# Performance work log

Hardware: AMD Instinct MI355X
Metric: run time of the kernel (lower is better)

Reference implementation:

```python
import jax, jax.numpy as jnp
import numpy as np


def setup_inputs() -> dict:
    key = jax.random.key(0)
    ka, kb = jax.random.split(key)
    a = jax.random.normal(ka, (16384, 3), dtype=jnp.float32)
    b = jax.random.normal(kb, (16384, 3), dtype=jnp.float32)
    return {"a": a, "b": b}


def reference(a, b):
    # Pairwise squared L2 via the expansion ||a-b||^2 = ||a||^2 + ||b||^2 - 2 a.b,
    # avoiding materializing the [N, M, D] diff tensor the torch code builds.
    a2 = jnp.sum(a * a, axis=-1)                      # [N]
    b2 = jnp.sum(b * b, axis=-1)                      # [M]
    cross = jnp.einsum("nd,md->nm", a, b)             # [N, M]
    d2 = a2[:, None] + b2[None, :] - 2.0 * cross       # [N, M]
    dist = jnp.sqrt(jnp.maximum(d2, 0.0))              # clamp for numerical safety
    min_dist = jnp.min(dist, axis=1)                   # [N] nearest-neighbor dist
    return jnp.sum(min_dist)
```

## Files before the change

kernel.cpp:

```cpp
#include <hip/hip_runtime.h>
#include <math.h>


#define NPTS 16384

typedef short s16x8 __attribute__((ext_vector_type(8)));
typedef unsigned int u32x4 __attribute__((ext_vector_type(4)));
typedef float f32x16 __attribute__((ext_vector_type(16)));

__device__ __forceinline__ unsigned short f2bf(float x) {
    unsigned u = __float_as_uint(x);
    u = u + 0x7FFFu + ((u >> 16) & 1u);
    return (unsigned short)(u >> 16);
}
__device__ __forceinline__ float bf2f(unsigned short h) {
    return __uint_as_float((unsigned)h << 16);
}
__device__ __forceinline__ unsigned pk(unsigned short lo, unsigned short hi) {
    return (unsigned)lo | ((unsigned)hi << 16);
}

__global__ __launch_bounds__(256)
void cd_packb_kernel(const float* __restrict__ b,
                     u32x4* __restrict__ bcmp) {
    const int i = blockIdx.x * 256 + threadIdx.x;
    const float x = b[3 * i + 0], y = b[3 * i + 1], z = b[3 * i + 2];
    const float n2 = fmaf(x, x, fmaf(y, y, z * z));
    const unsigned short hx = f2bf(x), hy = f2bf(y), hz = f2bf(z);
    const unsigned short thx = f2bf(-2.0f * bf2f(hx));
    const unsigned short thy = f2bf(-2.0f * bf2f(hy));
    const unsigned short thz = f2bf(-2.0f * bf2f(hz));
    const unsigned short tlx = f2bf(-2.0f * (x - bf2f(hx)));
    const unsigned short tly = f2bf(-2.0f * (y - bf2f(hy)));
    const unsigned short tlz = f2bf(-2.0f * (z - bf2f(hz)));
    const unsigned short n2h = f2bf(n2), n2l = f2bf(n2 - bf2f(n2h));
    bcmp[i] = (u32x4){ pk(thx, thy), pk(thz, tlx), pk(tly, tlz), pk(n2h, n2l) };
}

__device__ __forceinline__ s16x8 make_afrag(const float* __restrict__ a,
                                            int row, int khalf) {
    const float x = a[3 * row + 0];
    const float y = a[3 * row + 1];
    const float z = a[3 * row + 2];
    const float n2 = fmaf(x, x, fmaf(y, y, z * z));
    const unsigned short hx = f2bf(x), hy = f2bf(y), hz = f2bf(z);
    const unsigned short lx = f2bf(x - bf2f(hx));
    const unsigned short ly = f2bf(y - bf2f(hy));
    const unsigned short lz = f2bf(z - bf2f(hz));
    const unsigned short n2h = f2bf(n2);
    const unsigned short n2l = f2bf(n2 - bf2f(n2h));
    const unsigned short one = 0x3F80u;
    const s16x8 lo = {(short)hx, (short)hy, (short)hz, (short)hx,
                      (short)hy, (short)hz, (short)lx, (short)ly};
    const s16x8 hi = {(short)lz, (short)lx, (short)ly, (short)lz,
                      (short)n2h, (short)n2l, (short)one, (short)one};
    return khalf ? hi : lo;
}

__global__ __launch_bounds__(512, 4)
void cd_sweep_kernel(const float* __restrict__ a,
                     const u32x4* __restrict__ bcmp,
                     float* __restrict__ gmin) {
    __shared__ float red[8][64];
    const int tid   = threadIdx.x;
    const int lane  = tid & 63;
    const int wave  = tid >> 6;
    const int col   = lane & 31;
    const int khalf = lane >> 5;
    const int agroup = blockIdx.x >> 1;
    const int g      = blockIdx.x & 1;

    const s16x8 af0 = make_afrag(a, agroup * 64 + col, khalf);
    const s16x8 af1 = make_afrag(a, agroup * 64 + 32 + col, khalf);

    f32x16 best0, best1, zero;
    #pragma unroll
    for (int r = 0; r < 16; ++r) {
        best0[r] = 3.4028235e38f; best1[r] = 3.4028235e38f; zero[r] = 0.0f;
    }

    const unsigned Kone = 0x3F803F80u;
    const u32x4* bp = bcmp + g * 8192 + wave * 1024 + col;

    #define EXPAND(e, d)                           \
        e[0] = khalf ? d[1] : d[0];                \
        e[1] = khalf ? d[2] : d[1];                \
        e[2] = khalf ? Kone : d[2];                \
        e[3] = khalf ? d[3] : d[0];

    #pragma unroll 2
    for (int t = 0; t < 32; t += 2) {
        const u32x4 d0 = bp[(t + 0) * 32];
        const u32x4 d1 = bp[(t + 1) * 32];
        u32x4 e0, e1;
        EXPAND(e0, d0) EXPAND(e1, d1)
        {
            const f32x16 c0 = __builtin_amdgcn_mfma_f32_32x32x16_bf16(
                __builtin_bit_cast(s16x8, e0), af0, zero, 0, 0, 0);
            const f32x16 c1 = __builtin_amdgcn_mfma_f32_32x32x16_bf16(
                __builtin_bit_cast(s16x8, e1), af0, zero, 0, 0, 0);
            #pragma unroll
            for (int r = 0; r < 16; ++r)
                best0[r] = fminf(fminf(c0[r], c1[r]), best0[r]);
        }
        {
            const f32x16 c0 = __builtin_amdgcn_mfma_f32_32x32x16_bf16(
                __builtin_bit_cast(s16x8, e0), af1, zero, 0, 0, 0);
            const f32x16 c1 = __builtin_amdgcn_mfma_f32_32x32x16_bf16(
                __builtin_bit_cast(s16x8, e1), af1, zero, 0, 0, 0);
            #pragma unroll
            for (int r = 0; r < 16; ++r)
                best1[r] = fminf(fminf(c0[r], c1[r]), best1[r]);
        }
    }
    #undef EXPAND

    float m0 = best0[0], m1 = best1[0];
    #pragma unroll
    for (int r = 1; r < 16; ++r) {
        m0 = fminf(m0, best0[r]);
        m1 = fminf(m1, best1[r]);
    }
    m0 = fminf(m0, __shfl_xor(m0, 32, 64));
    m1 = fminf(m1, __shfl_xor(m1, 32, 64));

    if (lane < 32) {
        red[wave][col]      = m0;
        red[wave][col + 32] = m1;
    }
    __syncthreads();
    if (tid < 64) {
        float v = red[0][tid];
        #pragma unroll
        for (int w = 1; w < 8; ++w) v = fminf(v, red[w][tid]);
        gmin[g * NPTS + agroup * 64 + tid] = fmaxf(v, 0.0f);
    }
}

__global__ __launch_bounds__(1024)
void cd_reduce_kernel(const float* __restrict__ gmin,
                      float* __restrict__ out) {
    __shared__ float red[16];
    const int tid = threadIdx.x;
    const float4* g0 = (const float4*)gmin;
    const float4* g1 = (const float4*)(gmin + NPTS);

    float s = 0.0f;
    #pragma unroll
    for (int i = tid; i < NPTS / 4; i += 1024) {
        const float4 u = g0[i];
        const float4 v = g1[i];
        s += sqrtf(fminf(u.x, v.x)) + sqrtf(fminf(u.y, v.y)) +
             sqrtf(fminf(u.z, v.z)) + sqrtf(fminf(u.w, v.w));
    }
    for (int off = 32; off > 0; off >>= 1)
        s += __shfl_down(s, off, 64);
    if ((tid & 63) == 0) red[tid >> 6] = s;
    __syncthreads();
    if (tid == 0) {
        float t = 0.0f;
        #pragma unroll
        for (int w = 0; w < 16; ++w) t += red[w];
        out[0] = t;
    }
}

extern "C" void kernel_launch(void* const* d_in, const int* in_sizes, int n_in,
                              void* d_out, int out_size, void* d_ws, size_t ws_size,
                              hipStream_t stream) {
    const float* a = (const float*)d_in[0];
    const float* b = (const float*)d_in[1];
    float* out = (float*)d_out;
    char* ws = (char*)d_ws;
    const size_t tail = (ws_size >= (1u << 20)) ? (ws_size - (512u << 10)) : 0u;
    u32x4* bcmp = (u32x4*)(ws + tail);
    float* gmin = (float*)(ws + tail + 256 * 1024);

    cd_packb_kernel<<<NPTS / 256, 256, 0, stream>>>(b, bcmp);
    cd_sweep_kernel<<<NPTS / 32, 512, 0, stream>>>(a, bcmp, gmin);
    cd_reduce_kernel<<<1, 1024, 0, stream>>>(gmin, out);
}
```

Measured before the change: 69.68 us.

## Fuse pack, sweep and reduce into one cooperative kernel with grid syncs

Replaces the three-launch pipeline (pack B, MFMA sweep, final reduce) with a single cooperative kernel of 256 blocks × 1024 threads. Each block packs a 64-point slice of B, waits at a grid-wide sync, sweeps all of B for its 64 A rows, then syncs again so block 0 can do the sqrt-sum. The goal is to remove launch overhead and the inter-kernel gaps. In exchange it pays for two grid barriers and runs one large block per CU instead of more, smaller blocks, which may cut latency hiding. If the cooperative launch fails, it falls back to the original three kernels.

```diff
diff --git a/kernel.cpp b/kernel.cpp
--- a/kernel.cpp
+++ b/kernel.cpp
@@ -1,8 +1,11 @@
 #include <hip/hip_runtime.h>
+#include <hip/hip_cooperative_groups.h>
 #include <math.h>
 
 
 #define NPTS 16384
+
+namespace cg = cooperative_groups;
 
 typedef short s16x8 __attribute__((ext_vector_type(8)));
 typedef unsigned int u32x4 __attribute__((ext_vector_type(4)));
@@ -20,10 +23,7 @@
     return (unsigned)lo | ((unsigned)hi << 16);
 }
 
-__global__ __launch_bounds__(256)
-void cd_packb_kernel(const float* __restrict__ b,
-                     u32x4* __restrict__ bcmp) {
-    const int i = blockIdx.x * 256 + threadIdx.x;
+__device__ __forceinline__ u32x4 make_bcmp(const float* __restrict__ b, int i) {
     const float x = b[3 * i + 0], y = b[3 * i + 1], z = b[3 * i + 2];
     const float n2 = fmaf(x, x, fmaf(y, y, z * z));
     const unsigned short hx = f2bf(x), hy = f2bf(y), hz = f2bf(z);
@@ -34,7 +34,7 @@
     const unsigned short tly = f2bf(-2.0f * (y - bf2f(hy)));
     const unsigned short tlz = f2bf(-2.0f * (z - bf2f(hz)));
     const unsigned short n2h = f2bf(n2), n2l = f2bf(n2 - bf2f(n2h));
-    bcmp[i] = (u32x4){ pk(thx, thy), pk(thz, tlx), pk(tly, tlz), pk(n2h, n2l) };
+    return (u32x4){ pk(thx, thy), pk(thz, tlx), pk(tly, tlz), pk(n2h, n2l) };
 }
 
 __device__ __forceinline__ s16x8 make_afrag(const float* __restrict__ a,
@@ -57,6 +57,119 @@
     return khalf ? hi : lo;
 }
 
+#define EXPAND(e, d)                           \
+    e[0] = khalf ? d[1] : d[0];                \
+    e[1] = khalf ? d[2] : d[1];                \
+    e[2] = khalf ? Kone : d[2];                \
+    e[3] = khalf ? d[3] : d[0];
+
+__global__ __launch_bounds__(1024, 4)
+void cd_fused_kernel(const float* __restrict__ a,
+                     const float* __restrict__ b,
+                     u32x4* __restrict__ bcmp,
+                     float* __restrict__ gmin,
+                     float* __restrict__ out) {
+    __shared__ float red[16][64];
+    const int tid   = threadIdx.x;
+    const int lane  = tid & 63;
+    const int wave  = tid >> 6;
+    const int col   = lane & 31;
+    const int khalf = lane >> 5;
+
+    const s16x8 af0 = make_afrag(a, blockIdx.x * 64 + col, khalf);
+    const s16x8 af1 = make_afrag(a, blockIdx.x * 64 + 32 + col, khalf);
+
+    if (tid < 64) {
+        const int i = blockIdx.x * 64 + tid;
+        bcmp[i] = make_bcmp(b, i);
+    }
+    cg::this_grid().sync();
+
+    f32x16 best0, best1, zero;
+    #pragma unroll
+    for (int r = 0; r < 16; ++r) {
+        best0[r] = 3.4028235e38f; best1[r] = 3.4028235e38f; zero[r] = 0.0f;
+    }
+
+    const unsigned Kone = 0x3F803F80u;
+    const u32x4* bp = bcmp + wave * 1024 + col;
+
+    #pragma unroll 2
+    for (int t = 0; t < 32; t += 2) {
+        const u32x4 d0 = bp[(t + 0) * 32];
+        const u32x4 d1 = bp[(t + 1) * 32];
+        u32x4 e0, e1;
+        EXPAND(e0, d0) EXPAND(e1, d1)
+        {
+            const f32x16 c0 = __builtin_amdgcn_mfma_f32_32x32x16_bf16(
+                __builtin_bit_cast(s16x8, e0), af0, zero, 0, 0, 0);
+            const f32x16 c1 = __builtin_amdgcn_mfma_f32_32x32x16_bf16(
+                __builtin_bit_cast(s16x8, e1), af0, zero, 0, 0, 0);
+            #pragma unroll
+            for (int r = 0; r < 16; ++r)
+                best0[r] = fminf(fminf(c0[r], c1[r]), best0[r]);
+        }
+        {
+            const f32x16 c0 = __builtin_amdgcn_mfma_f32_32x32x16_bf16(
+                __builtin_bit_cast(s16x8, e0), af1, zero, 0, 0, 0);
+            const f32x16 c1 = __builtin_amdgcn_mfma_f32_32x32x16_bf16(
+                __builtin_bit_cast(s16x8, e1), af1, zero, 0, 0, 0);
+            #pragma unroll
+            for (int r = 0; r < 16; ++r)
+                best1[r] = fminf(fminf(c0[r], c1[r]), best1[r]);
+        }
+    }
+
+    float m0 = best0[0], m1 = best1[0];
+    #pragma unroll
+    for (int r = 1; r < 16; ++r) {
+        m0 = fminf(m0, best0[r]);
+        m1 = fminf(m1, best1[r]);
+    }
+    m0 = fminf(m0, __shfl_xor(m0, 32, 64));
+    m1 = fminf(m1, __shfl_xor(m1, 32, 64));
+
+    if (lane < 32) {
+        red[wave][col]      = m0;
+        red[wave][col + 32] = m1;
+    }
+    __syncthreads();
+    if (tid < 64) {
+        float v = red[0][tid];
+        #pragma unroll
+        for (int w = 1; w < 16; ++w) v = fminf(v, red[w][tid]);
+        gmin[blockIdx.x * 64 + tid] = fmaxf(v, 0.0f);
+    }
+    cg::this_grid().sync();
+
+    if (blockIdx.x == 0) {
+        const float4* g4 = (const float4*)gmin;
+        float s = 0.0f;
+        #pragma unroll
+        for (int i = tid; i < NPTS / 4; i += 1024) {
+            const float4 v = g4[i];
+            s += sqrtf(v.x) + sqrtf(v.y) + sqrtf(v.z) + sqrtf(v.w);
+        }
+        for (int off = 32; off > 0; off >>= 1)
+            s += __shfl_down(s, off, 64);
+        if ((tid & 63) == 0) red[0][tid >> 6] = s;
+        __syncthreads();
+        if (tid == 0) {
+            float t = 0.0f;
+            #pragma unroll
+            for (int w = 0; w < 16; ++w) t += red[0][w];
+            out[0] = t;
+        }
+    }
+}
+
+__global__ __launch_bounds__(256)
+void cd_packb_kernel(const float* __restrict__ b,
+                     u32x4* __restrict__ bcmp) {
+    const int i = blockIdx.x * 256 + threadIdx.x;
+    bcmp[i] = make_bcmp(b, i);
+}
+
 __global__ __launch_bounds__(512, 4)
 void cd_sweep_kernel(const float* __restrict__ a,
                      const u32x4* __restrict__ bcmp,
@@ -78,15 +191,8 @@
     for (int r = 0; r < 16; ++r) {
         best0[r] = 3.4028235e38f; best1[r] = 3.4028235e38f; zero[r] = 0.0f;
     }
-
     const unsigned Kone = 0x3F803F80u;
     const u32x4* bp = bcmp + g * 8192 + wave * 1024 + col;
-
-    #define EXPAND(e, d)                           \
-        e[0] = khalf ? d[1] : d[0];                \
-        e[1] = khalf ? d[2] : d[1];                \
-        e[2] = khalf ? Kone : d[2];                \
-        e[3] = khalf ? d[3] : d[0];
 
     #pragma unroll 2
     for (int t = 0; t < 32; t += 2) {
@@ -113,7 +219,6 @@
                 best1[r] = fminf(fminf(c0[r], c1[r]), best1[r]);
         }
     }
-    #undef EXPAND
 
     float m0 = best0[0], m1 = best1[0];
     #pragma unroll
@@ -138,8 +243,8 @@
 }
 
 __global__ __launch_bounds__(1024)
-void cd_reduce_kernel(const float* __restrict__ gmin,
-                      float* __restrict__ out) {
+void cd_reduce2_kernel(const float* __restrict__ gmin,
+                       float* __restrict__ out) {
     __shared__ float red[16];
     const int tid = threadIdx.x;
     const float4* g0 = (const float4*)gmin;
@@ -176,7 +281,13 @@
     u32x4* bcmp = (u32x4*)(ws + tail);
     float* gmin = (float*)(ws + tail + 256 * 1024);
 
-    cd_packb_kernel<<<NPTS / 256, 256, 0, stream>>>(b, bcmp);
-    cd_sweep_kernel<<<NPTS / 32, 512, 0, stream>>>(a, bcmp, gmin);
-    cd_reduce_kernel<<<1, 1024, 0, stream>>>(gmin, out);
-}
+    void* args[5] = { (void*)&a, (void*)&b, (void*)&bcmp, (void*)&gmin, (void*)&out };
+    const hipError_t e = hipLaunchCooperativeKernel(
+        reinterpret_cast<const void*>(&cd_fused_kernel),
+        dim3(256), dim3(1024), args, 0, stream);
+    if (e != hipSuccess) {
+        cd_packb_kernel<<<NPTS / 256, 256, 0, stream>>>(b, bcmp);
+        cd_sweep_kernel<<<NPTS / 32, 512, 0, stream>>>(a, bcmp, gmin);
+        cd_reduce2_kernel<<<1, 1024, 0, stream>>>(gmin, out);
+    }
+}
```

New measurement: 128.9 us. 1.85x slower.

## Fuse final reduction into sweep via last-block atomic and widen blocks to 1024 threads

Applied to the files above, without the earlier changes.

The sweep kernel now uses 1024-thread blocks covering all of B per 64-row A group, which removes the two-way B split and the cross-split min. The final sqrt-and-sum reduction is moved into the last finishing block, detected with an atomic counter that the pack kernel resets, so the separate reduce launch goes away. The inner loop is unrolled by four loads per iteration. The grid shrinks from 512 to 256 blocks, which may underfill the GPU's compute units, and the last block's serial tail reduction adds latency.

```diff
diff --git a/kernel.cpp b/kernel.cpp
--- a/kernel.cpp
+++ b/kernel.cpp
@@ -20,10 +20,7 @@
     return (unsigned)lo | ((unsigned)hi << 16);
 }
 
-__global__ __launch_bounds__(256)
-void cd_packb_kernel(const float* __restrict__ b,
-                     u32x4* __restrict__ bcmp) {
-    const int i = blockIdx.x * 256 + threadIdx.x;
+__device__ __forceinline__ u32x4 make_bcmp(const float* __restrict__ b, int i) {
     const float x = b[3 * i + 0], y = b[3 * i + 1], z = b[3 * i + 2];
     const float n2 = fmaf(x, x, fmaf(y, y, z * z));
     const unsigned short hx = f2bf(x), hy = f2bf(y), hz = f2bf(z);
@@ -34,7 +31,7 @@
     const unsigned short tly = f2bf(-2.0f * (y - bf2f(hy)));
     const unsigned short tlz = f2bf(-2.0f * (z - bf2f(hz)));
     const unsigned short n2h = f2bf(n2), n2l = f2bf(n2 - bf2f(n2h));
-    bcmp[i] = (u32x4){ pk(thx, thy), pk(thz, tlx), pk(tly, tlz), pk(n2h, n2l) };
+    return (u32x4){ pk(thx, thy), pk(thz, tlx), pk(tly, tlz), pk(n2h, n2l) };
 }
 
 __device__ __forceinline__ s16x8 make_afrag(const float* __restrict__ a,
@@ -57,21 +54,37 @@
     return khalf ? hi : lo;
 }
 
-__global__ __launch_bounds__(512, 4)
+#define EXPAND(e, d)                           \
+    e[0] = khalf ? d[1] : d[0];                \
+    e[1] = khalf ? d[2] : d[1];                \
+    e[2] = khalf ? Kone : d[2];                \
+    e[3] = khalf ? d[3] : d[0];
+
+__global__ __launch_bounds__(256)
+void cd_packb_kernel(const float* __restrict__ b,
+                     u32x4* __restrict__ bcmp,
+                     unsigned int* __restrict__ done) {
+    const int i = blockIdx.x * 256 + threadIdx.x;
+    bcmp[i] = make_bcmp(b, i);
+    if (i == 0) *done = 0u;
+}
+
+__global__ __launch_bounds__(1024, 4)
 void cd_sweep_kernel(const float* __restrict__ a,
                      const u32x4* __restrict__ bcmp,
-                     float* __restrict__ gmin) {
-    __shared__ float red[8][64];
+                     float* __restrict__ gmin,
+                     unsigned int* __restrict__ done,
+                     float* __restrict__ out) {
+    __shared__ float red[16][64];
+    __shared__ int isLast;
     const int tid   = threadIdx.x;
     const int lane  = tid & 63;
     const int wave  = tid >> 6;
     const int col   = lane & 31;
     const int khalf = lane >> 5;
-    const int agroup = blockIdx.x >> 1;
-    const int g      = blockIdx.x & 1;
-
-    const s16x8 af0 = make_afrag(a, agroup * 64 + col, khalf);
-    const s16x8 af1 = make_afrag(a, agroup * 64 + 32 + col, khalf);
+
+    const s16x8 af0 = make_afrag(a, blockIdx.x * 64 + col, khalf);
+    const s16x8 af1 = make_afrag(a, blockIdx.x * 64 + 32 + col, khalf);
 
     f32x16 best0, best1, zero;
     #pragma unroll
@@ -80,18 +93,13 @@
     }
 
     const unsigned Kone = 0x3F803F80u;
-    const u32x4* bp = bcmp + g * 8192 + wave * 1024 + col;
-
-    #define EXPAND(e, d)                           \
-        e[0] = khalf ? d[1] : d[0];                \
-        e[1] = khalf ? d[2] : d[1];                \
-        e[2] = khalf ? Kone : d[2];                \
-        e[3] = khalf ? d[3] : d[0];
-
-    #pragma unroll 2
-    for (int t = 0; t < 32; t += 2) {
+    const u32x4* bp = bcmp + wave * 1024 + col;
+
+    for (int t = 0; t < 32; t += 4) {
         const u32x4 d0 = bp[(t + 0) * 32];
         const u32x4 d1 = bp[(t + 1) * 32];
+        const u32x4 d2 = bp[(t + 2) * 32];
+        const u32x4 d3 = bp[(t + 3) * 32];
         u32x4 e0, e1;
         EXPAND(e0, d0) EXPAND(e1, d1)
         {
@@ -112,8 +120,27 @@
             for (int r = 0; r < 16; ++r)
                 best1[r] = fminf(fminf(c0[r], c1[r]), best1[r]);
         }
-    }
-    #undef EXPAND
+        u32x4 e2, e3;
+        EXPAND(e2, d2) EXPAND(e3, d3)
+        {
+            const f32x16 c0 = __builtin_amdgcn_mfma_f32_32x32x16_bf16(
+                __builtin_bit_cast(s16x8, e2), af0, zero, 0, 0, 0);
+            const f32x16 c1 = __builtin_amdgcn_mfma_f32_32x32x16_bf16(
+                __builtin_bit_cast(s16x8, e3), af0, zero, 0, 0, 0);
+            #pragma unroll
+            for (int r = 0; r < 16; ++r)
+                best0[r] = fminf(fminf(c0[r], c1[r]), best0[r]);
+        }
+        {
+            const f32x16 c0 = __builtin_amdgcn_mfma_f32_32x32x16_bf16(
+                __builtin_bit_cast(s16x8, e2), af1, zero, 0, 0, 0);
+            const f32x16 c1 = __builtin_amdgcn_mfma_f32_32x32x16_bf16(
+                __builtin_bit_cast(s16x8, e3), af1, zero, 0, 0, 0);
+            #pragma unroll
+            for (int r = 0; r < 16; ++r)
+                best1[r] = fminf(fminf(c0[r], c1[r]), best1[r]);
+        }
+    }
 
     float m0 = best0[0], m1 = best1[0];
     #pragma unroll
@@ -132,36 +159,38 @@
     if (tid < 64) {
         float v = red[0][tid];
         #pragma unroll
-        for (int w = 1; w < 8; ++w) v = fminf(v, red[w][tid]);
-        gmin[g * NPTS + agroup * 64 + tid] = fmaxf(v, 0.0f);
-    }
-}
-
-__global__ __launch_bounds__(1024)
-void cd_reduce_kernel(const float* __restrict__ gmin,
-                      float* __restrict__ out) {
-    __shared__ float red[16];
-    const int tid = threadIdx.x;
-    const float4* g0 = (const float4*)gmin;
-    const float4* g1 = (const float4*)(gmin + NPTS);
-
-    float s = 0.0f;
-    #pragma unroll
-    for (int i = tid; i < NPTS / 4; i += 1024) {
-        const float4 u = g0[i];
-        const float4 v = g1[i];
-        s += sqrtf(fminf(u.x, v.x)) + sqrtf(fminf(u.y, v.y)) +
-             sqrtf(fminf(u.z, v.z)) + sqrtf(fminf(u.w, v.w));
-    }
-    for (int off = 32; off > 0; off >>= 1)
-        s += __shfl_down(s, off, 64);
-    if ((tid & 63) == 0) red[tid >> 6] = s;
+        for (int w = 1; w < 16; ++w) v = fminf(v, red[w][tid]);
+        gmin[blockIdx.x * 64 + tid] = fmaxf(v, 0.0f);
+        __threadfence();
+    }
     __syncthreads();
     if (tid == 0) {
-        float t = 0.0f;
+        const unsigned old = atomicAdd(done, 1u);
+        isLast = (old == 255u);
+    }
+    __syncthreads();
+    if (!isLast) return;
+
+    __threadfence();
+    {
+        const float4* g4 = (const float4*)gmin;
+        float s = 0.0f;
         #pragma unroll
-        for (int w = 0; w < 16; ++w) t += red[w];
-        out[0] = t;
+        for (int i = tid; i < NPTS / 4; i += 1024) {
+            const float4 v = g4[i];
+            s += sqrtf(v.x) + sqrtf(v.y) + sqrtf(v.z) + sqrtf(v.w);
+        }
+        for (int off = 32; off > 0; off >>= 1)
+            s += __shfl_down(s, off, 64);
+        __syncthreads();
+        if ((tid & 63) == 0) red[0][tid >> 6] = s;
+        __syncthreads();
+        if (tid == 0) {
+            float t = 0.0f;
+            #pragma unroll
+            for (int w = 0; w < 16; ++w) t += red[0][w];
+            out[0] = t;
+        }
     }
 }
 
@@ -175,8 +204,8 @@
     const size_t tail = (ws_size >= (1u << 20)) ? (ws_size - (512u << 10)) : 0u;
     u32x4* bcmp = (u32x4*)(ws + tail);
     float* gmin = (float*)(ws + tail + 256 * 1024);
-
-    cd_packb_kernel<<<NPTS / 256, 256, 0, stream>>>(b, bcmp);
-    cd_sweep_kernel<<<NPTS / 32, 512, 0, stream>>>(a, bcmp, gmin);
-    cd_reduce_kernel<<<1, 1024, 0, stream>>>(gmin, out);
-}
+    unsigned int* done = (unsigned int*)(ws + tail + 320 * 1024);
+
+    cd_packb_kernel<<<NPTS / 256, 256, 0, stream>>>(b, bcmp, done);
+    cd_sweep_kernel<<<256, 1024, 0, stream>>>(a, bcmp, gmin, done, out);
+}
```

Result: slower. 76.86 us (+10.3%).
